# Kernel optimization log

Measured on AMD Instinct MI355X. Metric: run time of the kernel, lower is better.

## Reference

```python
import jax, jax.numpy as jnp
import numpy as np

DIM = 1024
NUM_HEADS = 16
HEAD_DIM = DIM // NUM_HEADS  # 64
SCALE = float(np.sqrt(HEAD_DIM))


def setup_inputs() -> dict:
    key = jax.random.key(0)
    k1, k2, k3, k4 = jax.random.split(key, 4)
    B, N = 2, 2048
    x = jax.random.normal(k1, (B, N, DIM), dtype=jnp.float32)
    # torch nn.Linear weights are [out_features, in_features]
    w_qkv = jax.random.normal(k2, (3 * DIM, DIM), dtype=jnp.float32) * (1.0 / np.sqrt(DIM))
    w_proj = jax.random.normal(k3, (DIM, DIM), dtype=jnp.float32) * (1.0 / np.sqrt(DIM))
    b_proj = jax.random.normal(k4, (DIM,), dtype=jnp.float32) * 0.02
    return {"x": x, "w_qkv": w_qkv, "w_proj": w_proj, "b_proj": b_proj}


def reference(x, w_qkv, w_proj, b_proj):
    B, N, C = x.shape
    H, D = NUM_HEADS, HEAD_DIM
    # qkv linear (no bias): [B,N,3C]
    qkv = jnp.einsum('bnc,oc->bno', x, w_qkv)
    qkv = qkv.reshape(B, N, 3, H, D).transpose(2, 0, 3, 1, 4)  # [3,B,H,N,D]
    q, k, v = qkv[0], qkv[1], qkv[2]
    attn = jnp.einsum('bhnd,bhmd->bhnm', q, k) / SCALE  # [B,H,N,N]
    attn = jax.nn.softmax(attn, axis=-1)
    out = jnp.einsum('bhnm,bhmd->bhnd', attn, v)  # [B,H,N,D]
    out = out.transpose(0, 2, 1, 3).reshape(B, N, C)
    return jnp.einsum('bnc,oc->bno', out, w_proj) + b_proj
```

## Files before the change

### kernel.cpp

```cpp
#include <hip/hip_runtime.h>


typedef __bf16 bf16x8 __attribute__((ext_vector_type(8)));
typedef __bf16 bf16x4 __attribute__((ext_vector_type(4)));
typedef float f32x4 __attribute__((ext_vector_type(4)));

#define NTOK 2048
#define MFMA16(a, b, c) __builtin_amdgcn_mfma_f32_16x16x32_bf16((a), (b), (c), 0, 0, 0)

__device__ __forceinline__ unsigned short f2bf(float f) {
    unsigned int u = __float_as_uint(f);
    u = (u + 0x7FFFu + ((u >> 16) & 1u)) >> 16;
    return (unsigned short)u;
}

__device__ __forceinline__ float hw_exp2(float x) {
#if __has_builtin(__builtin_amdgcn_exp2f)
    return __builtin_amdgcn_exp2f(x);
#else
    float r;
    asm("v_exp_f32 %0, %1" : "=v"(r) : "v"(x));
    return r;
#endif
}

__device__ __forceinline__ void gload16(const void* g, void* l) {
    __builtin_amdgcn_global_load_lds(
        (__attribute__((address_space(1))) void*)(g),
        (__attribute__((address_space(3))) void*)(l), 16, 0, 0);
}

__global__ __launch_bounds__(256) void cast3_kernel(
    const float* __restrict__ x, const float* __restrict__ wq,
    const float* __restrict__ wp, unsigned short* __restrict__ xb,
    unsigned short* __restrict__ wqb, unsigned short* __restrict__ wpb) {
    const int NX = 1048576, NWQ = 786432;
    int i = blockIdx.x * 256 + threadIdx.x;
    const float* src;
    unsigned short* dst;
    int j;
    if (i < NX) { src = x; dst = xb; j = i; }
    else if (i < NX + NWQ) { src = wq; dst = wqb; j = i - NX; }
    else { src = wp; dst = wpb; j = i - NX - NWQ; }
    const float4 v = reinterpret_cast<const float4*>(src)[j];
    ushort4 o;
    o.x = f2bf(v.x); o.y = f2bf(v.y); o.z = f2bf(v.z); o.w = f2bf(v.w);
    reinterpret_cast<ushort4*>(dst)[j] = o;
}

template <int EPI>
__global__ __launch_bounds__(512) void gemm_bt_kernel(
    const unsigned short* __restrict__ A, const unsigned short* __restrict__ B,
    int K, int Ncols,
    unsigned short* __restrict__ q_out, unsigned short* __restrict__ k_out,
    unsigned short* __restrict__ vt_out,
    float* __restrict__ c_out, const float* __restrict__ bias) {
    __shared__ __align__(16) char smem[32768];
    const int tid = threadIdx.x;
    const int l = tid & 63;
    const int wid = tid >> 6;
    const int c = l & 15, g = l >> 4;
    const int wr = wid >> 2, wc = wid & 3;
    const int m0 = blockIdx.x * 128, n0 = blockIdx.y * 128;

    f32x4 acc[4][2] = {};

    const int srow = tid >> 2;
    const int sc16 = (tid & 3) ^ (srow & 3);
    auto STAGE = [&](int buf, int kt) {
        gload16(A + (size_t)(m0 + srow) * K + kt + sc16 * 8,
                smem + buf * 8192 + wid * 1024);
        gload16(B + (size_t)(n0 + srow) * K + kt + sc16 * 8,
                smem + 16384 + buf * 8192 + wid * 1024);
    };

    STAGE(0, 0);
    __syncthreads();

    const int NK = K >> 5;
    int cur = 0;
    for (int ki = 0; ki < NK; ++ki) {
        if (ki + 1 < NK) STAGE(cur ^ 1, (ki + 1) * 32);
        bf16x8 af[4], bfr[2];
#pragma unroll
        for (int m = 0; m < 4; ++m) {
            const int row = wr * 64 + m * 16 + c;
            const int c16 = g ^ (row & 3);
            af[m] = *(const bf16x8*)(smem + cur * 8192 + row * 64 + c16 * 16);
        }
#pragma unroll
        for (int n = 0; n < 2; ++n) {
            const int row = wc * 32 + n * 16 + c;
            const int c16 = g ^ (row & 3);
            bfr[n] = *(const bf16x8*)(smem + 16384 + cur * 8192 + row * 64 + c16 * 16);
        }
#pragma unroll
        for (int m = 0; m < 4; ++m)
#pragma unroll
            for (int n = 0; n < 2; ++n)
                acc[m][n] = MFMA16(af[m], bfr[n], acc[m][n]);
        __syncthreads();
        cur ^= 1;
    }

    if (EPI == 0 && n0 >= 2048) {
#pragma unroll
        for (int m = 0; m < 4; ++m) {
            const int tl0 = wr * 64 + m * 16 + g * 4;
#pragma unroll
            for (int n = 0; n < 2; ++n) {
                const int oc = wc * 32 + n * 16 + c;
                bf16x4 pv;
#pragma unroll
                for (int r = 0; r < 4; ++r) pv[r] = (__bf16)acc[m][n][r];
                *(bf16x4*)(smem + oc * 256 + ((tl0 * 2) ^ ((oc & 7) << 4))) = pv;
            }
        }
        __syncthreads();
        const int b = m0 >> 11;
        const int mloc = m0 & 2047;
#pragma unroll
        for (int qq = 0; qq < 4; ++qq) {
            const int ci = qq * 512 + tid;
            const int oc = ci >> 4, j16 = ci & 15;
            const int o = n0 + oc;
            const int head = b * 16 + ((o >> 6) & 15), d = o & 63;
            const bf16x4* src = (const bf16x4*)(smem + oc * 256 +
                                                ((j16 * 16) ^ ((oc & 7) << 4)));
            const int tl8 = j16 * 8;
            const int tpb = (tl8 & ~63) | (tl8 & 0x20) | ((tl8 & 0x10) >> 2) |
                            ((tl8 & 0x08) << 1);
            unsigned short* orow = vt_out + ((size_t)head * 64 + d) * NTOK + mloc;
            *(bf16x4*)(orow + tpb) = src[0];
            *(bf16x4*)(orow + tpb + 8) = src[1];
        }
        return;
    }

#pragma unroll
    for (int m = 0; m < 4; ++m) {
        const int gmb = m0 + wr * 64 + m * 16 + (g << 2);
#pragma unroll
        for (int n = 0; n < 2; ++n) {
            const int gn = n0 + wc * 32 + n * 16 + c;
            if (EPI == 0) {
                const int which = gn >> 10;
                const int h = (gn >> 6) & 15, d = gn & 63;
#pragma unroll
                for (int r = 0; r < 4; ++r) {
                    const int gm = gmb + r;
                    const int head = ((gm >> 11) << 4) | h;
                    const int t = gm & 2047;
                    const float v = acc[m][n][r];
                    if (which == 0)
                        q_out[((size_t)head * NTOK + t) * 64 + d] =
                            f2bf(v * 0.18033688011f);
                    else
                        k_out[((size_t)head * NTOK + t) * 64 + d] = f2bf(v);
                }
            } else {
                const float bv = bias[gn];
#pragma unroll
                for (int r = 0; r < 4; ++r)
                    c_out[(size_t)(gmb + r) * Ncols + gn] = acc[m][n][r] + bv;
            }
        }
    }
}

__global__ __launch_bounds__(256) void attn_kernel(
    const unsigned short* __restrict__ Qb, const unsigned short* __restrict__ Kb,
    const unsigned short* __restrict__ Vt, unsigned short* __restrict__ Ob) {
    __shared__ __align__(16) unsigned short ldsK[2][64 * 64];
    __shared__ __align__(16) unsigned short ldsV[2][64 * 64];

    const int tid = threadIdx.x, l = tid & 63, wid = tid >> 6;
    const int c = l & 15, g = l >> 4;
    const int head = blockIdx.x;
    const int q0 = blockIdx.y * 128 + wid * 32;

    const unsigned short* Qh = Qb + (size_t)head * NTOK * 64;
    const unsigned short* Kh = Kb + (size_t)head * NTOK * 64;
    const unsigned short* Vh = Vt + (size_t)head * 64 * NTOK;

    bf16x8 qf[2][2];
#pragma unroll
    for (int mq = 0; mq < 2; ++mq)
#pragma unroll
        for (int kk = 0; kk < 2; ++kk)
            qf[mq][kk] = *(const bf16x8*)(Qh + (size_t)(q0 + mq * 16 + c) * 64 +
                                          kk * 32 + g * 8);

    f32x4 o_acc[2][4] = {};
    f32x4 lsum[2] = {};

    const int srow = tid >> 3;

    auto STAGE = [&](int buf, int kbase) {
#pragma unroll
        for (int r = 0; r < 2; ++r) {
            const int row = r * 32 + srow;
            const int slot = (tid & 7) ^ (row & 7);
            gload16(Kh + (size_t)(kbase + row) * 64 + slot * 8,
                    (char*)ldsK[buf] + wid * 1024 + r * 4096);
            gload16(Vh + (size_t)row * NTOK + kbase + slot * 8,
                    (char*)ldsV[buf] + wid * 1024 + r * 4096);
        }
    };

    STAGE(0, 0);
    __syncthreads();

    int cur = 0;
    for (int it = 0; it < 32; ++it) {
        if (it + 1 < 32) STAGE(cur ^ 1, (it + 1) * 64);

        f32x4 s0[4] = {}, s1[4] = {};
#pragma unroll
        for (int mk = 0; mk < 4; ++mk) {
            const int row = mk * 16 + c;
#pragma unroll
            for (int kk = 0; kk < 2; ++kk) {
                const int slot = (kk * 4 + g) ^ (row & 7);
                const bf16x8 kf =
                    *(const bf16x8*)((const char*)ldsK[cur] + row * 128 + slot * 16);
                s0[mk] = MFMA16(kf, qf[0][kk], s0[mk]);
                s1[mk] = MFMA16(kf, qf[1][kk], s1[mk]);
            }
        }

        bf16x8 pkw0[2], pkw1[2];
#pragma unroll
        for (int mk = 0; mk < 4; ++mk) {
            const int kv = mk >> 1, hh = (mk & 1) * 4;
            {
                const float p0 = hw_exp2(s0[mk][0]);
                const float p1 = hw_exp2(s0[mk][1]);
                const float p2 = hw_exp2(s0[mk][2]);
                const float p3 = hw_exp2(s0[mk][3]);
                lsum[0][0] += p0; lsum[0][1] += p1; lsum[0][2] += p2; lsum[0][3] += p3;
                pkw0[kv][hh + 0] = (__bf16)p0; pkw0[kv][hh + 1] = (__bf16)p1;
                pkw0[kv][hh + 2] = (__bf16)p2; pkw0[kv][hh + 3] = (__bf16)p3;
            }
            {
                const float p0 = hw_exp2(s1[mk][0]);
                const float p1 = hw_exp2(s1[mk][1]);
                const float p2 = hw_exp2(s1[mk][2]);
                const float p3 = hw_exp2(s1[mk][3]);
                lsum[1][0] += p0; lsum[1][1] += p1; lsum[1][2] += p2; lsum[1][3] += p3;
                pkw1[kv][hh + 0] = (__bf16)p0; pkw1[kv][hh + 1] = (__bf16)p1;
                pkw1[kv][hh + 2] = (__bf16)p2; pkw1[kv][hh + 3] = (__bf16)p3;
            }
        }

#pragma unroll
        for (int dm = 0; dm < 4; ++dm) {
            const int row = dm * 16 + c;
#pragma unroll
            for (int kv = 0; kv < 2; ++kv) {
                const int slot = (kv * 4 + g) ^ (row & 7);
                const bf16x8 vt =
                    *(const bf16x8*)((const char*)ldsV[cur] + row * 128 + slot * 16);
                o_acc[0][dm] = MFMA16(vt, pkw0[kv], o_acc[0][dm]);
                o_acc[1][dm] = MFMA16(vt, pkw1[kv], o_acc[1][dm]);
            }
        }
        __syncthreads();
        cur ^= 1;
    }

    const int b = head >> 4, h = head & 15;
#pragma unroll
    for (int mq = 0; mq < 2; ++mq) {
        float lr = (lsum[mq][0] + lsum[mq][1]) + (lsum[mq][2] + lsum[mq][3]);
        lr += __shfl_xor(lr, 16);
        lr += __shfl_xor(lr, 32);
        const float inv = 1.f / lr;
        unsigned short* orow =
            Ob + ((size_t)b * NTOK + q0 + mq * 16 + c) * 1024 + h * 64;
#pragma unroll
        for (int dm = 0; dm < 4; ++dm) {
            bf16x4 ov;
#pragma unroll
            for (int r = 0; r < 4; ++r) ov[r] = (__bf16)(o_acc[mq][dm][r] * inv);
            *(bf16x4*)(orow + dm * 16 + g * 4) = ov;
        }
    }
}

extern "C" void kernel_launch(void* const* d_in, const int* in_sizes, int n_in,
                              void* d_out, int out_size, void* d_ws, size_t ws_size,
                              hipStream_t stream) {
    const float* x = (const float*)d_in[0];
    const float* w_qkv = (const float*)d_in[1];
    const float* w_proj = (const float*)d_in[2];
    const float* b_proj = (const float*)d_in[3];
    float* out = (float*)d_out;

    char* ws = (char*)d_ws;
    const size_t MB = 1 << 20;
    unsigned short* xb = (unsigned short*)(ws);
    unsigned short* wqkvb = (unsigned short*)(ws + 8 * MB);
    unsigned short* wpb = (unsigned short*)(ws + 14 * MB);
    unsigned short* Qb = (unsigned short*)(ws + 16 * MB);
    unsigned short* Kb = (unsigned short*)(ws + 24 * MB);
    unsigned short* Vt = (unsigned short*)(ws + 32 * MB);
    unsigned short* attnb = xb;

    cast3_kernel<<<8192, 256, 0, stream>>>(x, w_qkv, w_proj, xb, wqkvb, wpb);

    gemm_bt_kernel<0><<<dim3(32, 24), 512, 0, stream>>>(
        xb, wqkvb, 1024, 3072, Qb, Kb, Vt, nullptr, nullptr);

    attn_kernel<<<dim3(32, 16), 256, 0, stream>>>(Qb, Kb, Vt, attnb);

    gemm_bt_kernel<1><<<dim3(32, 8), 512, 0, stream>>>(
        attnb, wpb, 1024, 1024, nullptr, nullptr, nullptr, out, b_proj);
}
```

Baseline: 114.2 us.

## Split attention KV range in two and add a combine kernel

The attention kernel now splits the 2048-key range into two halves along a third grid dimension, doubling the block count. Each half writes unnormalized bf16 partial outputs and fp32 row sums to separate buffers. A new combine kernel adds the two partials and divides by the summed row totals before the output projection. The aim is more parallelism and better latency hiding on the GPU, in exchange for an extra kernel launch, extra global-memory traffic, and bf16 rounding of the unnormalized partials.

Measured after the change: 122.9 us. 1.08x slower.

```diff
diff --git a/kernel.cpp b/kernel.cpp
--- a/kernel.cpp
+++ b/kernel.cpp
@@ -170,7 +170,9 @@
 
 __global__ __launch_bounds__(256) void attn_kernel(
     const unsigned short* __restrict__ Qb, const unsigned short* __restrict__ Kb,
-    const unsigned short* __restrict__ Vt, unsigned short* __restrict__ Ob) {
+    const unsigned short* __restrict__ Vt,
+    unsigned short* __restrict__ op0, unsigned short* __restrict__ op1,
+    float* __restrict__ lpart) {
     __shared__ __align__(16) unsigned short ldsK[2][64 * 64];
     __shared__ __align__(16) unsigned short ldsV[2][64 * 64];
 
@@ -178,6 +180,8 @@
     const int c = l & 15, g = l >> 4;
     const int head = blockIdx.x;
     const int q0 = blockIdx.y * 128 + wid * 32;
+    const int split = blockIdx.z;
+    const int kv0 = split * 1024;
 
     const unsigned short* Qh = Qb + (size_t)head * NTOK * 64;
     const unsigned short* Kh = Kb + (size_t)head * NTOK * 64;
@@ -208,12 +212,12 @@
         }
     };
 
-    STAGE(0, 0);
+    STAGE(0, kv0);
     __syncthreads();
 
     int cur = 0;
-    for (int it = 0; it < 32; ++it) {
-        if (it + 1 < 32) STAGE(cur ^ 1, (it + 1) * 64);
+    for (int it = 0; it < 16; ++it) {
+        if (it + 1 < 16) STAGE(cur ^ 1, kv0 + (it + 1) * 64);
 
         f32x4 s0[4] = {}, s1[4] = {};
 #pragma unroll
@@ -270,22 +274,43 @@
     }
 
     const int b = head >> 4, h = head & 15;
+    unsigned short* op = split ? op1 : op0;
 #pragma unroll
     for (int mq = 0; mq < 2; ++mq) {
         float lr = (lsum[mq][0] + lsum[mq][1]) + (lsum[mq][2] + lsum[mq][3]);
         lr += __shfl_xor(lr, 16);
         lr += __shfl_xor(lr, 32);
-        const float inv = 1.f / lr;
+        if (g == 0)
+            lpart[(split << 16) + (head << 11) + q0 + mq * 16 + c] = lr;
         unsigned short* orow =
-            Ob + ((size_t)b * NTOK + q0 + mq * 16 + c) * 1024 + h * 64;
+            op + ((size_t)b * NTOK + q0 + mq * 16 + c) * 1024 + h * 64;
 #pragma unroll
         for (int dm = 0; dm < 4; ++dm) {
             bf16x4 ov;
 #pragma unroll
-            for (int r = 0; r < 4; ++r) ov[r] = (__bf16)(o_acc[mq][dm][r] * inv);
+            for (int r = 0; r < 4; ++r) ov[r] = (__bf16)o_acc[mq][dm][r];
             *(bf16x4*)(orow + dm * 16 + g * 4) = ov;
         }
     }
+}
+
+__global__ __launch_bounds__(256) void combine_kernel(
+    const unsigned short* __restrict__ p0, const unsigned short* __restrict__ p1,
+    const float* __restrict__ lp, unsigned short* __restrict__ out) {
+    const int i = blockIdx.x * 256 + threadIdx.x;
+    const int t = i >> 7;
+    const int col = (i & 127) * 8;
+    const int head = ((t >> 11) << 4) | (col >> 6);
+    const int q = t & 2047;
+    const float lv = lp[(head << 11) + q] + lp[(1 << 16) + (head << 11) + q];
+    const float inv = 1.f / lv;
+    const bf16x8 a = *(const bf16x8*)(p0 + (size_t)i * 8);
+    const bf16x8 b = *(const bf16x8*)(p1 + (size_t)i * 8);
+    bf16x8 o;
+#pragma unroll
+    for (int j = 0; j < 8; ++j)
+        o[j] = (__bf16)(((float)a[j] + (float)b[j]) * inv);
+    *(bf16x8*)(out + (size_t)i * 8) = o;
 }
 
 extern "C" void kernel_launch(void* const* d_in, const int* in_sizes, int n_in,
@@ -305,6 +330,9 @@
     unsigned short* Qb = (unsigned short*)(ws + 16 * MB);
     unsigned short* Kb = (unsigned short*)(ws + 24 * MB);
     unsigned short* Vt = (unsigned short*)(ws + 32 * MB);
+    unsigned short* op1 = (unsigned short*)(ws + 40 * MB);
+    float* lpart = (float*)(ws + 48 * MB);
+    unsigned short* op0 = xb;
     unsigned short* attnb = xb;
 
     cast3_kernel<<<8192, 256, 0, stream>>>(x, w_qkv, w_proj, xb, wqkvb, wpb);
@@ -312,7 +340,9 @@
     gemm_bt_kernel<0><<<dim3(32, 24), 512, 0, stream>>>(
         xb, wqkvb, 1024, 3072, Qb, Kb, Vt, nullptr, nullptr);
 
-    attn_kernel<<<dim3(32, 16), 256, 0, stream>>>(Qb, Kb, Vt, attnb);
+    attn_kernel<<<dim3(32, 16, 2), 256, 0, stream>>>(Qb, Kb, Vt, op0, op1, lpart);
+
+    combine_kernel<<<2048, 256, 0, stream>>>(op0, op1, lpart, attnb);
 
     gemm_bt_kernel<1><<<dim3(32, 8), 512, 0, stream>>>(
         attnb, wpb, 1024, 1024, nullptr, nullptr, nullptr, out, b_proj);
```

## Triple-buffer LDS staging with vmcnt waits in GEMM and attention kernels

Applied to the files above, without the earlier changes.

Both the GEMM and attention kernels move from double-buffered to triple-buffered LDS staging, prefetching two tiles ahead. Each full __syncthreads is replaced by an explicit s_waitcnt vmcnt(N) plus a barrier, so only the oldest outstanding tile must land before compute starts. The aim is to hide more global-load latency and keep just one barrier per iteration. In exchange, LDS use grows by half in each kernel, which may lower occupancy.

Measured after the change: 108.6 us. 1.05x faster.

```diff
diff --git a/kernel.cpp b/kernel.cpp
--- a/kernel.cpp
+++ b/kernel.cpp
@@ -7,6 +7,11 @@
 
 #define NTOK 2048
 #define MFMA16(a, b, c) __builtin_amdgcn_mfma_f32_16x16x32_bf16((a), (b), (c), 0, 0, 0)
+
+#define WAITBAR(N)                                         \
+    asm volatile("s_waitcnt vmcnt(" #N ")" ::: "memory"); \
+    __builtin_amdgcn_s_barrier();                          \
+    __builtin_amdgcn_sched_barrier(0)
 
 __device__ __forceinline__ unsigned short f2bf(float f) {
     unsigned int u = __float_as_uint(f);
@@ -55,7 +60,7 @@
     unsigned short* __restrict__ q_out, unsigned short* __restrict__ k_out,
     unsigned short* __restrict__ vt_out,
     float* __restrict__ c_out, const float* __restrict__ bias) {
-    __shared__ __align__(16) char smem[32768];
+    __shared__ __align__(16) char smem[49152];
     const int tid = threadIdx.x;
     const int l = tid & 63;
     const int wid = tid >> 6;
@@ -67,43 +72,53 @@
 
     const int srow = tid >> 2;
     const int sc16 = (tid & 3) ^ (srow & 3);
-    auto STAGE = [&](int buf, int kt) {
+    auto STAGE = [&](int bi, int kt) {
         gload16(A + (size_t)(m0 + srow) * K + kt + sc16 * 8,
-                smem + buf * 8192 + wid * 1024);
+                smem + bi * 8192 + wid * 1024);
         gload16(B + (size_t)(n0 + srow) * K + kt + sc16 * 8,
-                smem + 16384 + buf * 8192 + wid * 1024);
+                smem + 24576 + bi * 8192 + wid * 1024);
     };
 
-    STAGE(0, 0);
-    __syncthreads();
-
-    const int NK = K >> 5;
-    int cur = 0;
-    for (int ki = 0; ki < NK; ++ki) {
-        if (ki + 1 < NK) STAGE(cur ^ 1, (ki + 1) * 32);
+    auto COMPUTE = [&](int bi) {
+        const char* bA = smem + bi * 8192;
+        const char* bB = smem + 24576 + bi * 8192;
         bf16x8 af[4], bfr[2];
 #pragma unroll
         for (int m = 0; m < 4; ++m) {
             const int row = wr * 64 + m * 16 + c;
-            const int c16 = g ^ (row & 3);
-            af[m] = *(const bf16x8*)(smem + cur * 8192 + row * 64 + c16 * 16);
+            af[m] = *(const bf16x8*)(bA + row * 64 + (g ^ (row & 3)) * 16);
         }
 #pragma unroll
         for (int n = 0; n < 2; ++n) {
             const int row = wc * 32 + n * 16 + c;
-            const int c16 = g ^ (row & 3);
-            bfr[n] = *(const bf16x8*)(smem + 16384 + cur * 8192 + row * 64 + c16 * 16);
+            bfr[n] = *(const bf16x8*)(bB + row * 64 + (g ^ (row & 3)) * 16);
         }
 #pragma unroll
         for (int m = 0; m < 4; ++m)
 #pragma unroll
             for (int n = 0; n < 2; ++n)
                 acc[m][n] = MFMA16(af[m], bfr[n], acc[m][n]);
+    };
+
+    const int NK = K >> 5;
+    STAGE(0, 0);
+    STAGE(1, 32);
+    int cb = 0, sb = 2;
+    for (int it = 0; it < NK - 2; ++it) {
+        WAITBAR(2);
+        STAGE(sb, (it + 2) * 32);
+        COMPUTE(cb);
+        cb = cb == 2 ? 0 : cb + 1;
+        sb = sb == 2 ? 0 : sb + 1;
+    }
+    WAITBAR(2);
+    COMPUTE(cb);
+    cb = cb == 2 ? 0 : cb + 1;
+    WAITBAR(0);
+    COMPUTE(cb);
+
+    if (EPI == 0 && n0 >= 2048) {
         __syncthreads();
-        cur ^= 1;
-    }
-
-    if (EPI == 0 && n0 >= 2048) {
 #pragma unroll
         for (int m = 0; m < 4; ++m) {
             const int tl0 = wr * 64 + m * 16 + g * 4;
@@ -171,8 +186,8 @@
 __global__ __launch_bounds__(256) void attn_kernel(
     const unsigned short* __restrict__ Qb, const unsigned short* __restrict__ Kb,
     const unsigned short* __restrict__ Vt, unsigned short* __restrict__ Ob) {
-    __shared__ __align__(16) unsigned short ldsK[2][64 * 64];
-    __shared__ __align__(16) unsigned short ldsV[2][64 * 64];
+    __shared__ __align__(16) unsigned short ldsK[3][64 * 64];
+    __shared__ __align__(16) unsigned short ldsV[3][64 * 64];
 
     const int tid = threadIdx.x, l = tid & 63, wid = tid >> 6;
     const int c = l & 15, g = l >> 4;
@@ -196,25 +211,21 @@
 
     const int srow = tid >> 3;
 
-    auto STAGE = [&](int buf, int kbase) {
+    auto STAGE = [&](int bi, int kbase) {
 #pragma unroll
         for (int r = 0; r < 2; ++r) {
             const int row = r * 32 + srow;
             const int slot = (tid & 7) ^ (row & 7);
             gload16(Kh + (size_t)(kbase + row) * 64 + slot * 8,
-                    (char*)ldsK[buf] + wid * 1024 + r * 4096);
+                    (char*)ldsK + bi * 8192 + wid * 1024 + r * 4096);
             gload16(Vh + (size_t)row * NTOK + kbase + slot * 8,
-                    (char*)ldsV[buf] + wid * 1024 + r * 4096);
+                    (char*)ldsV + bi * 8192 + wid * 1024 + r * 4096);
         }
     };
 
-    STAGE(0, 0);
-    __syncthreads();
-
-    int cur = 0;
-    for (int it = 0; it < 32; ++it) {
-        if (it + 1 < 32) STAGE(cur ^ 1, (it + 1) * 64);
-
+    auto COMPUTE = [&](int bi) {
+        const char* baseK = (const char*)ldsK + bi * 8192;
+        const char* baseV = (const char*)ldsV + bi * 8192;
         f32x4 s0[4] = {}, s1[4] = {};
 #pragma unroll
         for (int mk = 0; mk < 4; ++mk) {
@@ -222,13 +233,11 @@
 #pragma unroll
             for (int kk = 0; kk < 2; ++kk) {
                 const int slot = (kk * 4 + g) ^ (row & 7);
-                const bf16x8 kf =
-                    *(const bf16x8*)((const char*)ldsK[cur] + row * 128 + slot * 16);
+                const bf16x8 kf = *(const bf16x8*)(baseK + row * 128 + slot * 16);
                 s0[mk] = MFMA16(kf, qf[0][kk], s0[mk]);
                 s1[mk] = MFMA16(kf, qf[1][kk], s1[mk]);
             }
         }
-
         bf16x8 pkw0[2], pkw1[2];
 #pragma unroll
         for (int mk = 0; mk < 4; ++mk) {
@@ -252,22 +261,33 @@
                 pkw1[kv][hh + 2] = (__bf16)p2; pkw1[kv][hh + 3] = (__bf16)p3;
             }
         }
-
 #pragma unroll
         for (int dm = 0; dm < 4; ++dm) {
             const int row = dm * 16 + c;
 #pragma unroll
             for (int kv = 0; kv < 2; ++kv) {
                 const int slot = (kv * 4 + g) ^ (row & 7);
-                const bf16x8 vt =
-                    *(const bf16x8*)((const char*)ldsV[cur] + row * 128 + slot * 16);
+                const bf16x8 vt = *(const bf16x8*)(baseV + row * 128 + slot * 16);
                 o_acc[0][dm] = MFMA16(vt, pkw0[kv], o_acc[0][dm]);
                 o_acc[1][dm] = MFMA16(vt, pkw1[kv], o_acc[1][dm]);
             }
         }
-        __syncthreads();
-        cur ^= 1;
-    }
+    };
+
+    STAGE(0, 0);
+    STAGE(1, 64);
+    int cb = 0, sb = 2;
+    for (int it = 0; it < 30; ++it) {
+        WAITBAR(4);
+        STAGE(sb, (it + 2) * 64);
+        COMPUTE(cb);
+        cb = cb == 2 ? 0 : cb + 1;
+        sb = sb == 2 ? 0 : sb + 1;
+    }
+    WAITBAR(4);
+    COMPUTE(0);
+    WAITBAR(0);
+    COMPUTE(1);
 
     const int b = head >> 4, h = head & 15;
 #pragma unroll
```
